# Performance work log

Hardware: AMD Instinct MI355X
Metric: run time of the kernel (lower is better)

## Reference

```python
import jax, jax.numpy as jnp
import numpy as np

B, S, H = 2, 2048, 2048
NH, KVH, HD = 16, 4, 128
R = 16
LORA_SCALE = 32.0 / 16.0  # lora_alpha / lora_r
ATTN_SCALE = HD ** -0.5
NEG = -1e9


def setup_inputs() -> dict:
    key = jax.random.key(0)
    ks = jax.random.split(key, 16)
    q_dim, kv_dim = NH * HD, KVH * HD
    # RoPE tables
    inv_freq = 1.0 / (10000.0 ** (jnp.arange(0, HD, 2, dtype=jnp.float32) / HD))
    ang = jnp.arange(S, dtype=jnp.float32)[:, None] * inv_freq[None, :]  # [S, HD/2]
    emb = jnp.concatenate([ang, ang], axis=-1)  # [S, HD]
    cos = jnp.broadcast_to(jnp.cos(emb)[None], (B, S, HD))
    sin = jnp.broadcast_to(jnp.sin(emb)[None], (B, S, HD))
    # additive causal mask [B,1,S,S]
    causal = jnp.triu(jnp.full((S, S), NEG, dtype=jnp.float32), k=1)
    attention_mask = jnp.broadcast_to(causal[None, None], (B, 1, S, S))
    return {
        'hidden_states': jax.random.normal(ks[0], (B, S, H), jnp.float32),
        'cos': cos,
        'sin': sin,
        'attention_mask': attention_mask,
        'q_w': jax.random.normal(ks[1], (q_dim, H), jnp.float32) * 0.02,
        'k_w': jax.random.normal(ks[2], (kv_dim, H), jnp.float32) * 0.02,
        'v_w': jax.random.normal(ks[3], (kv_dim, H), jnp.float32) * 0.02,
        'q_b': jax.random.normal(ks[4], (q_dim,), jnp.float32) * 0.02,
        'k_b': jax.random.normal(ks[5], (kv_dim,), jnp.float32) * 0.02,
        'v_b': jax.random.normal(ks[6], (kv_dim,), jnp.float32) * 0.02,
        'q_A': jax.random.normal(ks[7], (H, R), jnp.float32) * (1.0 / np.sqrt(H)),
        'q_B': jax.random.normal(ks[8], (R, q_dim), jnp.float32) * 0.02,
        'k_A': jax.random.normal(ks[9], (H, R), jnp.float32) * (1.0 / np.sqrt(H)),
        'k_B': jax.random.normal(ks[10], (R, kv_dim), jnp.float32) * 0.02,
        'v_A': jax.random.normal(ks[11], (H, R), jnp.float32) * (1.0 / np.sqrt(H)),
        'v_B': jax.random.normal(ks[12], (R, kv_dim), jnp.float32) * 0.02,
        'o_w': jax.random.normal(ks[13], (H, H), jnp.float32) * 0.02,
    }


def _rotate_half(x):
    x1, x2 = x[..., : HD // 2], x[..., HD // 2:]
    return jnp.concatenate([-x2, x1], axis=-1)


def reference(hidden_states, cos, sin, attention_mask,
              q_w, k_w, v_w, q_b, k_b, v_b,
              q_A, q_B, k_A, k_B, v_A, v_B, o_w):
    x = hidden_states  # dropout p=0 (eval)
    # fused base + LoRA projections
    q = x @ q_w.T + q_b + LORA_SCALE * ((x @ q_A) @ q_B)  # [B,S,NH*HD]
    k = x @ k_w.T + k_b + LORA_SCALE * ((x @ k_A) @ k_B)  # [B,S,KVH*HD]
    v = x @ v_w.T + v_b + LORA_SCALE * ((x @ v_A) @ v_B)
    q = q.reshape(B, S, NH, HD).transpose(0, 2, 1, 3)   # [B,NH,S,HD]
    k = k.reshape(B, S, KVH, HD).transpose(0, 2, 1, 3)  # [B,KVH,S,HD]
    v = v.reshape(B, S, KVH, HD).transpose(0, 2, 1, 3)
    # RoPE
    c = cos[:, None]  # [B,1,S,HD]
    s = sin[:, None]
    q = q * c + _rotate_half(q) * s
    k = k * c + _rotate_half(k) * s
    # GQA: repeat kv heads
    n_rep = NH // KVH
    k = jnp.repeat(k, n_rep, axis=1)  # [B,NH,S,HD]
    v = jnp.repeat(v, n_rep, axis=1)
    scores = jnp.einsum('bhqd,bhkd->bhqk', q, k) * ATTN_SCALE
    scores = scores + attention_mask
    attn = jax.nn.softmax(scores.astype(jnp.float32), axis=-1).astype(q.dtype)
    out = jnp.einsum('bhqk,bhkd->bhqd', attn, v)
    out = out.transpose(0, 2, 1, 3).reshape(B, S, NH * HD)  # [B,S,H]
    return out @ o_w.T
```

## Files before the change

kernel.cpp:

```cpp
#include <hip/hip_runtime.h>

constexpr int cB   = 2;
constexpr int cS   = 2048;
constexpr int cH   = 2048;
constexpr int cNH  = 16;
constexpr int cKVH = 4;
constexpr int cHD  = 128;
constexpr int cQD  = 2048;
constexpr int cKVD = 512;
constexpr int cNQKV = 3072;
constexpr int cNTOK = 4096;
#define ATTN_SCALE 0.08838834764831845f
#define QSCALE 0.12751589549581288f

typedef __bf16 bf16;
typedef __attribute__((ext_vector_type(8))) __bf16 bf16x8;
typedef __attribute__((ext_vector_type(4))) __bf16 bf16x4;
typedef __attribute__((ext_vector_type(4))) float  f32x4;

__device__ __forceinline__ void async_load16(const bf16* g, bf16* l) {
    __builtin_amdgcn_global_load_lds(
        (const __attribute__((address_space(1))) void*)g,
        (__attribute__((address_space(3))) void*)l, 16, 0, 0);
}

__global__ __launch_bounds__(256) void prep_all(
        const float* __restrict__ x, bf16* __restrict__ Xbf,
        const float* __restrict__ ow, bf16* __restrict__ OWbf,
        const float* __restrict__ qw, const float* __restrict__ kw, const float* __restrict__ vw,
        const float* __restrict__ qA, const float* __restrict__ qB,
        const float* __restrict__ kA, const float* __restrict__ kB,
        const float* __restrict__ vA, const float* __restrict__ vB,
        const float* __restrict__ qb, const float* __restrict__ kbias, const float* __restrict__ vb,
        bf16* __restrict__ Wc, float* __restrict__ biasc) {
    const int bid = blockIdx.x;
    if (bid < 8192) {
        const int i = (bid * 256 + threadIdx.x) * 4;
        f32x4 v = *(const f32x4*)(x + i);
        bf16x4 o;
        o[0] = (bf16)v[0]; o[1] = (bf16)v[1]; o[2] = (bf16)v[2]; o[3] = (bf16)v[3];
        *(bf16x4*)(Xbf + i) = o;
        return;
    }
    if (bid < 12288) {
        const int i = ((bid - 8192) * 256 + threadIdx.x) * 4;
        f32x4 v = *(const f32x4*)(ow + i);
        bf16x4 o;
        o[0] = (bf16)v[0]; o[1] = (bf16)v[1]; o[2] = (bf16)v[2]; o[3] = (bf16)v[3];
        *(bf16x4*)(OWbf + i) = o;
        return;
    }
    const int pb = bid - 12288;
    const int bx = pb & 3, by = pb >> 2;
    const int wave = threadIdx.x >> 6, lane = threadIdx.x & 63;
    const int n = by * 4 + wave;
    const int k0 = bx * 512 + lane * 8;
    const float* W; const float* Am; const float* Bm; const float* bias; int nn, nd;
    if (n < cQD)             { W = qw; Am = qA; Bm = qB; bias = qb;    nn = n;               nd = cQD; }
    else if (n < cQD + cKVD) { W = kw; Am = kA; Bm = kB; bias = kbias; nn = n - cQD;         nd = cKVD; }
    else                     { W = vw; Am = vA; Bm = vB; bias = vb;    nn = n - cQD - cKVD;  nd = cKVD; }
    if (bx == 0 && lane == 0) biasc[n] = bias[nn];
    float bm[16];
    #pragma unroll
    for (int r = 0; r < 16; ++r) bm[r] = Bm[r * nd + nn];
    const float* wrow = W + (size_t)nn * cH + k0;
    f32x4 w0 = *(const f32x4*)(wrow);
    f32x4 w1 = *(const f32x4*)(wrow + 4);
    bf16x8 o;
    #pragma unroll
    for (int j = 0; j < 8; ++j) {
        const f32x4* am = (const f32x4*)(Am + (size_t)(k0 + j) * 16);
        f32x4 a0 = am[0], a1 = am[1], a2 = am[2], a3 = am[3];
        float acc = 0.f;
        #pragma unroll
        for (int c = 0; c < 4; ++c) acc += a0[c] * bm[c] + a1[c] * bm[4 + c]
                                         + a2[c] * bm[8 + c] + a3[c] * bm[12 + c];
        const float wv = (j < 4) ? w0[j] : w1[j - 4];
        o[j] = (bf16)(wv + 2.0f * acc);
    }
    *(bf16x8*)&Wc[(size_t)n * cH + k0] = o;
}

__global__ __launch_bounds__(256, 2) void gemm_qkv5(const bf16* __restrict__ A, const bf16* __restrict__ Bw,
                                                    const float* __restrict__ bias,
                                                    const float* __restrict__ cosb, const float* __restrict__ sinb,
                                                    bf16* __restrict__ Qr, bf16* __restrict__ Kr,
                                                    bf16* __restrict__ Vt) {
    __shared__ bf16 Al[128 * 128];
    __shared__ bf16 Bl[128 * 128];
    const int tid = threadIdx.x;
    const int wave = tid >> 6, lane = tid & 63;
    const int quad = lane >> 4, l16 = lane & 15;
    const int wr = wave >> 1, wc = wave & 1;
    const int K = cH;
    constexpr int GX = cNQKV / 128;
    constexpr int NWG = GX * (cNTOK / 128);

    const int orig = blockIdx.y * GX + blockIdx.x;
    const int swz = (orig & 7) * (NWG >> 3) + (orig >> 3);
    const long bm = (long)(swz / GX) * 128;
    const long bn = (long)(swz % GX) * 128;

    f32x4 acc[4][4];
    #pragma unroll
    for (int i = 0; i < 4; ++i)
        #pragma unroll
        for (int c = 0; c < 4; ++c) acc[i][c] = f32x4{0.f, 0.f, 0.f, 0.f};

    int ago[8], slo[8];
    #pragma unroll
    for (int i2 = 0; i2 < 8; ++i2) {
        const int si = i2 * 256 + tid;
        const int row = si >> 4, c16 = si & 15;
        const int csw = (c16 & 8) | ((c16 & 7) ^ (row & 7));
        ago[i2] = row * K + csw * 8;
        slo[i2] = si * 8;
    }
    const size_t bmK = (size_t)bm * K, bnK = (size_t)bn * K;

    auto STAGE = [&](int tt) {
        const bf16* As_ = A  + bmK + (size_t)tt * 128;
        const bf16* Bs_ = Bw + bnK + (size_t)tt * 128;
        #pragma unroll
        for (int i2 = 0; i2 < 8; ++i2) {
            async_load16(As_ + ago[i2], &Al[slo[i2]]);
            async_load16(Bs_ + ago[i2], &Bl[slo[i2]]);
        }
    };

    constexpr int NT = cH / 128;
    STAGE(0);
    const int sw = l16 & 7;

    for (int t = 0; t < NT; ++t) {
        asm volatile("s_waitcnt vmcnt(0)" ::: "memory");
        __builtin_amdgcn_s_barrier();
        #pragma unroll
        for (int ks = 0; ks < 4; ++ks) {
            const int g = ks * 4 + quad;
            const int gsw = (g & 8) | ((g & 7) ^ sw);
            const int cofs = gsw * 8;
            bf16x8 af[4], bfr[4];
            #pragma unroll
            for (int i = 0; i < 4; ++i)
                af[i] = *(const bf16x8*)&Al[(wr * 64 + i * 16 + l16) * 128 + cofs];
            #pragma unroll
            for (int c = 0; c < 4; ++c) {
                const int nrow = wc * 32 + (c & 1) * 16 + (c >> 1) * 64 + l16;
                bfr[c] = *(const bf16x8*)&Bl[nrow * 128 + cofs];
            }
            __builtin_amdgcn_s_setprio(1);
            #pragma unroll
            for (int i = 0; i < 4; ++i)
                #pragma unroll
                for (int c = 0; c < 4; ++c)
                    acc[i][c] = __builtin_amdgcn_mfma_f32_16x16x32_bf16(af[i], bfr[c], acc[i][c], 0, 0, 0);
            __builtin_amdgcn_s_setprio(0);
        }
        asm volatile("s_waitcnt lgkmcnt(0)" ::: "memory");
        __builtin_amdgcn_s_barrier();
        if (t + 1 < NT) STAGE(t + 1);
    }

    #pragma unroll
    for (int c = 0; c < 4; ++c) {
        const int nloc = wc * 32 + (c & 1) * 16 + (c >> 1) * 64 + l16;
        const float bv = bias[bn + nloc];
        #pragma unroll
        for (int i = 0; i < 4; ++i)
            #pragma unroll
            for (int r = 0; r < 4; ++r) acc[i][c][r] += bv;
    }

    const int head = (int)(bn >> 7);
    if (head < cNH + cKVH) {
        const bool isQ = head < cNH;
        #pragma unroll
        for (int cl = 0; cl < 2; ++cl) {
            const int d = wc * 32 + cl * 16 + l16;
            #pragma unroll
            for (int i = 0; i < 4; ++i)
                #pragma unroll
                for (int r = 0; r < 4; ++r) {
                    const long t = bm + wr * 64 + i * 16 + quad * 4 + r;
                    const float cv = cosb[t * cHD + d];
                    const float sv = sinb[t * cHD + d];
                    const float v1 = acc[i][cl][r], v2 = acc[i][cl + 2][r];
                    float o1 = v1 * cv - v2 * sv;
                    float o2 = v2 * cv + v1 * sv;
                    if (isQ) { o1 *= QSCALE; o2 *= QSCALE; }
                    const int b = (int)(t >> 11), s = (int)(t & 2047);
                    bf16* dst = isQ
                        ? Qr + ((size_t)(b * cNH + head) * cS + s) * cHD
                        : Kr + ((size_t)(b * cKVH + (head - cNH)) * cS + s) * cHD;
                    dst[d]      = (bf16)o1;
                    dst[d + 64] = (bf16)o2;
                }
        }
    } else {
        const int kv = head - cNH - cKVH;
        const int b = (int)(bm >> 11);
        const int sbase = (int)(bm & 2047);
        #pragma unroll
        for (int c = 0; c < 4; ++c) {
            const int d = wc * 32 + (c & 1) * 16 + (c >> 1) * 64 + l16;
            #pragma unroll
            for (int i = 0; i < 4; ++i) {
                const int s0 = sbase + wr * 64 + i * 16 + quad * 4;
                bf16x4 o4;
                #pragma unroll
                for (int r = 0; r < 4; ++r) o4[r] = (bf16)acc[i][c][r];
                *(bf16x4*)&Vt[((size_t)((b * cKVH + kv) * cHD) + d) * cS + s0] = o4;
            }
        }
    }
}

__global__ __launch_bounds__(256, 2) void gemm_oproj5(const bf16* __restrict__ A, const bf16* __restrict__ Bw,
                                                      float* __restrict__ Cp) {
    __shared__ bf16 Al[128 * 128];
    __shared__ bf16 Bl[128 * 128];
    const int tid = threadIdx.x;
    const int wave = tid >> 6, lane = tid & 63;
    const int quad = lane >> 4, l16 = lane & 15;
    const int wr = wave >> 1, wc = wave & 1;
    constexpr int K = cH, N = cH;
    constexpr int GX = cH / 128;
    constexpr int NWG = GX * (cNTOK / 128);

    const int orig = blockIdx.y * GX + blockIdx.x;
    const int swz = (orig & 7) * (NWG >> 3) + (orig >> 3);
    const long bm = (long)(swz / GX) * 128;
    const long bn = (long)(swz % GX) * 128;

    f32x4 acc[4][4];
    #pragma unroll
    for (int i = 0; i < 4; ++i)
        #pragma unroll
        for (int c = 0; c < 4; ++c) acc[i][c] = f32x4{0.f, 0.f, 0.f, 0.f};

    int ago[8], slo[8];
    #pragma unroll
    for (int i2 = 0; i2 < 8; ++i2) {
        const int si = i2 * 256 + tid;
        const int row = si >> 4, c16 = si & 15;
        const int csw = (c16 & 8) | ((c16 & 7) ^ (row & 7));
        ago[i2] = row * K + csw * 8;
        slo[i2] = si * 8;
    }
    const size_t bmK = (size_t)bm * K, bnK = (size_t)bn * K;

    auto STAGE = [&](int tt) {
        const bf16* As_ = A  + bmK + (size_t)tt * 128;
        const bf16* Bs_ = Bw + bnK + (size_t)tt * 128;
        #pragma unroll
        for (int i2 = 0; i2 < 8; ++i2) {
            async_load16(As_ + ago[i2], &Al[slo[i2]]);
            async_load16(Bs_ + ago[i2], &Bl[slo[i2]]);
        }
    };

    constexpr int NT = K / 128;
    STAGE(0);
    const int sw = l16 & 7;

    for (int t = 0; t < NT; ++t) {
        asm volatile("s_waitcnt vmcnt(0)" ::: "memory");
        __builtin_amdgcn_s_barrier();
        #pragma unroll
        for (int ks = 0; ks < 4; ++ks) {
            const int g = ks * 4 + quad;
            const int gsw = (g & 8) | ((g & 7) ^ sw);
            const int cofs = gsw * 8;
            bf16x8 af[4], bfr[4];
            #pragma unroll
            for (int i = 0; i < 4; ++i)
                af[i] = *(const bf16x8*)&Al[(wr * 64 + i * 16 + l16) * 128 + cofs];
            #pragma unroll
            for (int c = 0; c < 4; ++c)
                bfr[c] = *(const bf16x8*)&Bl[(wc * 64 + c * 16 + l16) * 128 + cofs];
            __builtin_amdgcn_s_setprio(1);
            #pragma unroll
            for (int i = 0; i < 4; ++i)
                #pragma unroll
                for (int c = 0; c < 4; ++c)
                    acc[i][c] = __builtin_amdgcn_mfma_f32_16x16x32_bf16(af[i], bfr[c], acc[i][c], 0, 0, 0);
            __builtin_amdgcn_s_setprio(0);
        }
        asm volatile("s_waitcnt lgkmcnt(0)" ::: "memory");
        __builtin_amdgcn_s_barrier();
        if (t + 1 < NT) STAGE(t + 1);
    }

    #pragma unroll
    for (int i = 0; i < 4; ++i)
        #pragma unroll
        for (int c = 0; c < 4; ++c) {
            const long m0 = bm + wr * 64 + i * 16 + quad * 4;
            const long n  = bn + wc * 64 + c * 16 + l16;
            #pragma unroll
            for (int r = 0; r < 4; ++r)
                Cp[(m0 + r) * N + n] = acc[i][c][r];
        }
}

__global__ __launch_bounds__(256, 2) void flash6(const bf16* __restrict__ Q, const bf16* __restrict__ K,
                                                 const bf16* __restrict__ Vt, bf16* __restrict__ Ob) {
    __shared__ bf16 kb[128 * 128];
    __shared__ bf16 vb[128 * 128];
    __shared__ bf16 pb[4 * 2048];
    const int tid = threadIdx.x;
    const int wave = tid >> 6, lane = tid & 63;
    const int quad = lane >> 4, l16 = lane & 15;
    const int pi = blockIdx.x;
    const int h = blockIdx.y, b = blockIdx.z;

    const bf16* Qh = Q  + (size_t)(b * cNH + h) * cS * cHD;
    const bf16* Kg = K  + (size_t)(b * cKVH + (h >> 2)) * cS * cHD;
    const bf16* Vg = Vt + (size_t)(b * cKVH + (h >> 2)) * cHD * cS;

    int kgo[8], vgo[8], slo[8];
    #pragma unroll
    for (int i2 = 0; i2 < 8; ++i2) {
        const int si = i2 * 256 + tid;
        const int row = si >> 4, c16 = si & 15;
        const int csw = (c16 & 8) | ((c16 & 7) ^ (row & 7));
        kgo[i2] = row * cHD + csw * 8;
        vgo[i2] = row * cS  + csw * 8;
        slo[i2] = si * 8;
    }

    #pragma unroll
    for (int t2 = 0; t2 < 2; ++t2) {
        const int qt = t2 == 0 ? (31 - pi) : pi;

        const bf16* Qg = Qh + (size_t)qt * 64 * cHD;
        bf16x8 qf[4];
        #pragma unroll
        for (int ks = 0; ks < 4; ++ks)
            qf[ks] = *(const bf16x8*)(Qg + (size_t)(wave * 16 + l16) * cHD + ks * 32 + quad * 8);

        f32x4 oac[8];
        #pragma unroll
        for (int dt = 0; dt < 8; ++dt) oac[dt] = f32x4{0.f, 0.f, 0.f, 0.f};
        float m_ = -3.0e38f, l_ = 0.f;

        const int nkt = (qt >> 1) + 1;
        for (int kt = 0; kt < nkt; ++kt) {
            __syncthreads();
            const bf16* Kt  = Kg + (size_t)kt * 128 * cHD;
            const bf16* Vtt = Vg + kt * 128;
            #pragma unroll
            for (int i2 = 0; i2 < 8; ++i2) async_load16(Kt + kgo[i2], kb + slo[i2]);
            #pragma unroll
            for (int i2 = 0; i2 < 8; ++i2) async_load16(Vtt + vgo[i2], vb + slo[i2]);
            __syncthreads();

            f32x4 st[8];
            #pragma unroll
            for (int mt = 0; mt < 8; ++mt) {
                bf16x8 kf[4];
                #pragma unroll
                for (int ks = 0; ks < 4; ++ks) {
                    const int c = ks * 4 + quad;
                    const int csw = (c & 8) | ((c & 7) ^ (l16 & 7));
                    kf[ks] = *(const bf16x8*)&kb[(mt * 16 + l16) * 128 + csw * 8];
                }
                f32x4 a = f32x4{0.f, 0.f, 0.f, 0.f};
                __builtin_amdgcn_s_setprio(1);
                #pragma unroll
                for (int ks = 0; ks < 4; ++ks)
                    a = __builtin_amdgcn_mfma_f32_16x16x32_bf16(kf[ks], qf[ks], a, 0, 0, 0);
                __builtin_amdgcn_s_setprio(0);
                st[mt] = a;
            }

            const int qpos = qt * 64 + wave * 16 + l16;
            float tmax = -3.0e38f;
            if ((kt * 128 + 127) > (qt * 64 + wave * 16)) {
                #pragma unroll
                for (int mt = 0; mt < 8; ++mt)
                    #pragma unroll
                    for (int r = 0; r < 4; ++r) {
                        const int kpos = kt * 128 + mt * 16 + quad * 4 + r;
                        if (kpos > qpos) st[mt][r] = -3.0e38f;
                        tmax = fmaxf(tmax, st[mt][r]);
                    }
            } else {
                #pragma unroll
                for (int mt = 0; mt < 8; ++mt)
                    #pragma unroll
                    for (int r = 0; r < 4; ++r) tmax = fmaxf(tmax, st[mt][r]);
            }
            tmax = fmaxf(tmax, __shfl_xor(tmax, 16, 64));
            tmax = fmaxf(tmax, __shfl_xor(tmax, 32, 64));
            const float mnew = fmaxf(m_, tmax);
            if (__any(tmax > m_)) {
                const float alpha = __builtin_amdgcn_exp2f(m_ - mnew);
                l_ *= alpha;
                #pragma unroll
                for (int dt = 0; dt < 8; ++dt)
                    #pragma unroll
                    for (int r = 0; r < 4; ++r) oac[dt][r] *= alpha;
            }
            m_ = mnew;
            float rs = 0.f;
            #pragma unroll
            for (int mt = 0; mt < 8; ++mt)
                #pragma unroll
                for (int r = 0; r < 4; ++r) {
                    const float p = __builtin_amdgcn_exp2f(st[mt][r] - mnew);
                    st[mt][r] = p;
                    rs += p;
                }
            rs += __shfl_xor(rs, 16, 64);
            rs += __shfl_xor(rs, 32, 64);
            l_ += rs;

            #pragma unroll
            for (int mt = 0; mt < 8; ++mt) {
                bf16x4 p4;
                #pragma unroll
                for (int r = 0; r < 4; ++r) p4[r] = (bf16)st[mt][r];
                const int c16 = mt * 2 + (quad >> 1);
                const int csw = (c16 & 8) | ((c16 & 7) ^ (l16 & 7));
                *(bf16x4*)&pb[wave * 2048 + l16 * 128 + csw * 8 + (quad & 1) * 4] = p4;
            }

            bf16x8 pf[4];
            #pragma unroll
            for (int ks = 0; ks < 4; ++ks) {
                const int c = ks * 4 + quad;
                const int csw = (c & 8) | ((c & 7) ^ (l16 & 7));
                pf[ks] = *(const bf16x8*)&pb[wave * 2048 + l16 * 128 + csw * 8];
            }
            #pragma unroll
            for (int dt = 0; dt < 8; ++dt) {
                bf16x8 vf[4];
                #pragma unroll
                for (int ks = 0; ks < 4; ++ks) {
                    const int c = ks * 4 + quad;
                    const int csw = (c & 8) | ((c & 7) ^ (l16 & 7));
                    vf[ks] = *(const bf16x8*)&vb[(dt * 16 + l16) * 128 + csw * 8];
                }
                __builtin_amdgcn_s_setprio(1);
                #pragma unroll
                for (int ks = 0; ks < 4; ++ks)
                    oac[dt] = __builtin_amdgcn_mfma_f32_16x16x32_bf16(vf[ks], pf[ks], oac[dt], 0, 0, 0);
                __builtin_amdgcn_s_setprio(0);
            }
        }

        const float inv = 1.0f / l_;
        const int token = qt * 64 + wave * 16 + l16;
        bf16* orow = Ob + (size_t)(b * cS + token) * (cNH * cHD) + h * cHD;
        #pragma unroll
        for (int dt = 0; dt < 8; ++dt) {
            bf16x4 o4;
            #pragma unroll
            for (int r = 0; r < 4; ++r) o4[r] = (bf16)(oac[dt][r] * inv);
            *(bf16x4*)&orow[dt * 16 + quad * 4] = o4;
        }
    }
}

extern "C" void kernel_launch(void* const* d_in, const int* in_sizes, int n_in,
                              void* d_out, int out_size, void* d_ws, size_t ws_size,
                              hipStream_t stream) {
    const float* x    = (const float*)d_in[0];
    const float* cosb = (const float*)d_in[1];
    const float* sinb = (const float*)d_in[2];
    const float* qw = (const float*)d_in[4];
    const float* kw = (const float*)d_in[5];
    const float* vw = (const float*)d_in[6];
    const float* qb = (const float*)d_in[7];
    const float* kb_ = (const float*)d_in[8];
    const float* vb = (const float*)d_in[9];
    const float* qA = (const float*)d_in[10];
    const float* qB = (const float*)d_in[11];
    const float* kA = (const float*)d_in[12];
    const float* kB = (const float*)d_in[13];
    const float* vA = (const float*)d_in[14];
    const float* vB = (const float*)d_in[15];
    const float* ow = (const float*)d_in[16];
    float* out = (float*)d_out;

    char* ws = (char*)d_ws;
    bf16* Xbf   = (bf16*)ws;  ws += (size_t)cNTOK * cH * 2;
    bf16* Wc    = (bf16*)ws;  ws += (size_t)cNQKV * cH * 2;
    float* biasc = (float*)ws; ws += (size_t)cNQKV * 4;
    bf16* Qr    = (bf16*)ws;  ws += (size_t)cB * cNH * cS * cHD * 2;
    bf16* Kr    = (bf16*)ws;  ws += (size_t)cB * cKVH * cS * cHD * 2;
    bf16* Vt    = (bf16*)ws;  ws += (size_t)cB * cKVH * cHD * cS * 2;
    bf16* OWbf  = (bf16*)ws;  ws += (size_t)cH * cH * 2;
    bf16* Aout  = (bf16*)ws;  ws += (size_t)cNTOK * cQD * 2;

    prep_all<<<15360, 256, 0, stream>>>(x, Xbf, ow, OWbf, qw, kw, vw, qA, qB, kA, kB, vA, vB,
                                        qb, kb_, vb, Wc, biasc);

    gemm_qkv5<<<dim3(cNQKV / 128, cNTOK / 128), 256, 0, stream>>>(Xbf, Wc, biasc, cosb, sinb, Qr, Kr, Vt);

    flash6<<<dim3(16, cNH, cB), 256, 0, stream>>>(Qr, Kr, Vt, Aout);

    gemm_oproj5<<<dim3(cH / 128, cNTOK / 128), 256, 0, stream>>>(Aout, OWbf, out);
}
```

Measured before the change: 372.8 us.

## Retile QKV GEMM to 256x128 blocks with 8 waves and K-step 64

The fused QKV projection GEMM moves from 128x128 tiles with 4 waves and a K-step of 128 to 256x128 tiles with 8 waves and a K-step of 64. The LDS footprint per block drops from 64KB to 48KB, and launch bounds are raised to 512 threads with 4 blocks per CU to increase occupancy. The larger M tile gives more reuse of each B tile. The change doubles the number of barrier-synchronised K iterations and halves the grid size, which may leave the CUs less evenly balanced.

```diff
diff --git a/kernel.cpp b/kernel.cpp
--- a/kernel.cpp
+++ b/kernel.cpp
@@ -81,24 +81,24 @@
     *(bf16x8*)&Wc[(size_t)n * cH + k0] = o;
 }
 
-__global__ __launch_bounds__(256, 2) void gemm_qkv5(const bf16* __restrict__ A, const bf16* __restrict__ Bw,
+__global__ __launch_bounds__(512, 4) void gemm_qkv6(const bf16* __restrict__ A, const bf16* __restrict__ Bw,
                                                     const float* __restrict__ bias,
                                                     const float* __restrict__ cosb, const float* __restrict__ sinb,
                                                     bf16* __restrict__ Qr, bf16* __restrict__ Kr,
                                                     bf16* __restrict__ Vt) {
-    __shared__ bf16 Al[128 * 128];
-    __shared__ bf16 Bl[128 * 128];
+    __shared__ bf16 Al[256 * 64];
+    __shared__ bf16 Bl[128 * 64];
     const int tid = threadIdx.x;
     const int wave = tid >> 6, lane = tid & 63;
     const int quad = lane >> 4, l16 = lane & 15;
-    const int wr = wave >> 1, wc = wave & 1;
+    const int wm = wave >> 1, wn = wave & 1;
     const int K = cH;
     constexpr int GX = cNQKV / 128;
-    constexpr int NWG = GX * (cNTOK / 128);
+    constexpr int NWG = GX * (cNTOK / 256);
 
     const int orig = blockIdx.y * GX + blockIdx.x;
     const int swz = (orig & 7) * (NWG >> 3) + (orig >> 3);
-    const long bm = (long)(swz / GX) * 128;
+    const long bm = (long)(swz / GX) * 256;
     const long bn = (long)(swz % GX) * 128;
 
     f32x4 acc[4][4];
@@ -107,28 +107,33 @@
         #pragma unroll
         for (int c = 0; c < 4; ++c) acc[i][c] = f32x4{0.f, 0.f, 0.f, 0.f};
 
-    int ago[8], slo[8];
-    #pragma unroll
-    for (int i2 = 0; i2 < 8; ++i2) {
-        const int si = i2 * 256 + tid;
-        const int row = si >> 4, c16 = si & 15;
-        const int csw = (c16 & 8) | ((c16 & 7) ^ (row & 7));
-        ago[i2] = row * K + csw * 8;
-        slo[i2] = si * 8;
+    int aago[4], aslo[4], bgo[2], bslo[2];
+    #pragma unroll
+    for (int i2 = 0; i2 < 4; ++i2) {
+        const int si = i2 * 512 + tid;
+        const int row = si >> 3, c8 = si & 7;
+        aago[i2] = row * K + (c8 ^ (row & 7)) * 8;
+        aslo[i2] = si * 8;
+    }
+    #pragma unroll
+    for (int i2 = 0; i2 < 2; ++i2) {
+        const int si = i2 * 512 + tid;
+        const int row = si >> 3, c8 = si & 7;
+        bgo[i2] = row * K + (c8 ^ (row & 7)) * 8;
+        bslo[i2] = si * 8;
     }
     const size_t bmK = (size_t)bm * K, bnK = (size_t)bn * K;
 
     auto STAGE = [&](int tt) {
-        const bf16* As_ = A  + bmK + (size_t)tt * 128;
-        const bf16* Bs_ = Bw + bnK + (size_t)tt * 128;
-        #pragma unroll
-        for (int i2 = 0; i2 < 8; ++i2) {
-            async_load16(As_ + ago[i2], &Al[slo[i2]]);
-            async_load16(Bs_ + ago[i2], &Bl[slo[i2]]);
-        }
+        const bf16* As_ = A  + bmK + (size_t)tt * 64;
+        const bf16* Bs_ = Bw + bnK + (size_t)tt * 64;
+        #pragma unroll
+        for (int i2 = 0; i2 < 4; ++i2) async_load16(As_ + aago[i2], &Al[aslo[i2]]);
+        #pragma unroll
+        for (int i2 = 0; i2 < 2; ++i2) async_load16(Bs_ + bgo[i2], &Bl[bslo[i2]]);
     };
 
-    constexpr int NT = cH / 128;
+    constexpr int NT = cH / 64;
     STAGE(0);
     const int sw = l16 & 7;
 
@@ -136,18 +141,17 @@
         asm volatile("s_waitcnt vmcnt(0)" ::: "memory");
         __builtin_amdgcn_s_barrier();
         #pragma unroll
-        for (int ks = 0; ks < 4; ++ks) {
+        for (int ks = 0; ks < 2; ++ks) {
             const int g = ks * 4 + quad;
-            const int gsw = (g & 8) | ((g & 7) ^ sw);
-            const int cofs = gsw * 8;
+            const int cofs = (g ^ sw) * 8;
             bf16x8 af[4], bfr[4];
             #pragma unroll
             for (int i = 0; i < 4; ++i)
-                af[i] = *(const bf16x8*)&Al[(wr * 64 + i * 16 + l16) * 128 + cofs];
+                af[i] = *(const bf16x8*)&Al[(wm * 64 + i * 16 + l16) * 64 + cofs];
             #pragma unroll
             for (int c = 0; c < 4; ++c) {
-                const int nrow = wc * 32 + (c & 1) * 16 + (c >> 1) * 64 + l16;
-                bfr[c] = *(const bf16x8*)&Bl[nrow * 128 + cofs];
+                const int nrow = wn * 32 + (c & 1) * 16 + (c >> 1) * 64 + l16;
+                bfr[c] = *(const bf16x8*)&Bl[nrow * 64 + cofs];
             }
             __builtin_amdgcn_s_setprio(1);
             #pragma unroll
@@ -164,7 +168,7 @@
 
     #pragma unroll
     for (int c = 0; c < 4; ++c) {
-        const int nloc = wc * 32 + (c & 1) * 16 + (c >> 1) * 64 + l16;
+        const int nloc = wn * 32 + (c & 1) * 16 + (c >> 1) * 64 + l16;
         const float bv = bias[bn + nloc];
         #pragma unroll
         for (int i = 0; i < 4; ++i)
@@ -177,12 +181,12 @@
         const bool isQ = head < cNH;
         #pragma unroll
         for (int cl = 0; cl < 2; ++cl) {
-            const int d = wc * 32 + cl * 16 + l16;
+            const int d = wn * 32 + cl * 16 + l16;
             #pragma unroll
             for (int i = 0; i < 4; ++i)
                 #pragma unroll
                 for (int r = 0; r < 4; ++r) {
-                    const long t = bm + wr * 64 + i * 16 + quad * 4 + r;
+                    const long t = bm + wm * 64 + i * 16 + quad * 4 + r;
                     const float cv = cosb[t * cHD + d];
                     const float sv = sinb[t * cHD + d];
                     const float v1 = acc[i][cl][r], v2 = acc[i][cl + 2][r];
@@ -203,10 +207,10 @@
         const int sbase = (int)(bm & 2047);
         #pragma unroll
         for (int c = 0; c < 4; ++c) {
-            const int d = wc * 32 + (c & 1) * 16 + (c >> 1) * 64 + l16;
+            const int d = wn * 32 + (c & 1) * 16 + (c >> 1) * 64 + l16;
             #pragma unroll
             for (int i = 0; i < 4; ++i) {
-                const int s0 = sbase + wr * 64 + i * 16 + quad * 4;
+                const int s0 = sbase + wm * 64 + i * 16 + quad * 4;
                 bf16x4 o4;
                 #pragma unroll
                 for (int r = 0; r < 4; ++r) o4[r] = (bf16)acc[i][c][r];
@@ -498,7 +502,7 @@
     prep_all<<<15360, 256, 0, stream>>>(x, Xbf, ow, OWbf, qw, kw, vw, qA, qB, kA, kB, vA, vB,
                                         qb, kb_, vb, Wc, biasc);
 
-    gemm_qkv5<<<dim3(cNQKV / 128, cNTOK / 128), 256, 0, stream>>>(Xbf, Wc, biasc, cosb, sinb, Qr, Kr, Vt);
+    gemm_qkv6<<<dim3(cNQKV / 128, cNTOK / 256), 512, 0, stream>>>(Xbf, Wc, biasc, cosb, sinb, Qr, Kr, Vt);
 
     flash6<<<dim3(16, cNH, cB), 256, 0, stream>>>(Qr, Kr, Vt, Aout);
 
```

After: 361.5 us. 3.0% less time.
